# Optimization experiments

Measured on AMD Instinct MI355X. Metric: run time of the kernel, lower is better.

## Reference

```python
import jax, jax.numpy as jnp
import numpy as np

NUM_EXPERTS = 8
TOP_K = 2
D = 512
F = 2048
B, L = 4, 1024


def setup_inputs() -> dict:
    key = jax.random.key(0)
    ks = jax.random.split(key, 5)
    std = D ** -0.5
    return {
        "x": jax.random.normal(ks[0], (B, L, D), jnp.float32),
        "gate_w": jax.random.normal(ks[1], (NUM_EXPERTS, D), jnp.float32) * std,
        "w1": jax.random.normal(ks[2], (NUM_EXPERTS, F, D), jnp.float32) * std,
        "w2": jax.random.normal(ks[3], (NUM_EXPERTS, D, F), jnp.float32) * (F ** -0.5),
        "w3": jax.random.normal(ks[4], (NUM_EXPERTS, F, D), jnp.float32) * std,
    }


def reference(x, gate_w, w1, w2, w3):
    b, l, d = x.shape
    xf = x.reshape(-1, d)                      # [T, D]
    T = xf.shape[0]
    router_logits = xf @ gate_w.T              # [T, E]
    # top-k routing in float32 (as in original), softmax over selected logits
    topk_w, topk_idx = jax.lax.top_k(router_logits.astype(jnp.float32), TOP_K)
    topk_w = jax.nn.softmax(topk_w, axis=-1).astype(x.dtype)  # [T, K]
    # combine weights per (token, expert): scatter top-k weights into dense [T, E]
    cw = jnp.zeros((T, NUM_EXPERTS), x.dtype)
    cw = cw.at[jnp.arange(T)[:, None], topk_idx].add(topk_w)
    # per-expert gated FFN (SiLU(x w1^T) * (x w3^T)) w2^T, batched over experts
    h = jax.nn.silu(jnp.einsum('td,efd->etf', xf, w1)) * jnp.einsum('td,efd->etf', xf, w3)
    y = jnp.einsum('etf,edf->etd', h, w2)      # [E, T, D]
    out = jnp.einsum('te,etd->td', cw, y)      # weighted combine
    return out.reshape(b, l, d), router_logits
```

## Files before the change

### kernel.cpp

```cpp
#include <hip/hip_runtime.h>

#define TTOK 4096
#define NEXP 8
#define DDIM 512
#define FDIM 2048
#define HROWS 8576

typedef __attribute__((ext_vector_type(8))) short short8;
typedef __attribute__((ext_vector_type(4))) float floatx4;

#define BAR()  __builtin_amdgcn_s_barrier()
#define SBAR() __builtin_amdgcn_sched_barrier(0)

__device__ __forceinline__ ushort f2b(float f) {
  unsigned u = __float_as_uint(f);
  u += 0x7fffu + ((u >> 16) & 1u);
  return (ushort)(u >> 16);
}

__device__ __forceinline__ void load16(void* lds, const void* g) {
  __builtin_amdgcn_global_load_lds(
      (const __attribute__((address_space(1))) unsigned int*)g,
      (__attribute__((address_space(3))) unsigned int*)lds, 16, 0, 0);
}


__global__ __launch_bounds__(256) void k_front(
    const float* __restrict__ x, const float* __restrict__ gw,
    float* __restrict__ logits, int* __restrict__ tok_e,
    float2* __restrict__ tok_w,
    const float* __restrict__ w1, ushort* __restrict__ w1t,
    const float* __restrict__ w3, ushort* __restrict__ w3t)
{
  __shared__ ushort sm[4096];
  const int tid = threadIdx.x;
  if (blockIdx.x < TTOK / 4) {
    const int lane = tid & 63;
    const int t = blockIdx.x * 4 + (tid >> 6);
    float xv[8];
#pragma unroll
    for (int i = 0; i < 8; ++i) xv[i] = x[(size_t)t * DDIM + lane + 64 * i];
    float lg[8];
#pragma unroll
    for (int e = 0; e < 8; ++e) {
      float a = 0.f;
#pragma unroll
      for (int i = 0; i < 8; ++i) a += xv[i] * gw[e * DDIM + lane + 64 * i];
#pragma unroll
      for (int s = 32; s; s >>= 1) a += __shfl_xor(a, s, 64);
      lg[e] = a;
    }
    if (lane < 8) logits[(size_t)t * 8 + lane] = lg[lane];
    if (lane == 0) {
      int i0 = 0; float v0 = lg[0];
#pragma unroll
      for (int e = 1; e < 8; ++e) { if (lg[e] > v0) { v0 = lg[e]; i0 = e; } }
      int i1 = -1; float v1 = -3.4e38f;
#pragma unroll
      for (int e = 0; e < 8; ++e) { if (e != i0 && lg[e] > v1) { v1 = lg[e]; i1 = e; } }
      float ex = expf(v1 - v0);
      float inv = 1.f / (1.f + ex);
      tok_e[t] = i0 | (i1 << 4);
      tok_w[t] = make_float2(inv, ex * inv);
    }
    return;
  }
  int bid = blockIdx.x - TTOK / 4;
  const float* src = (bid < 2048) ? w1 : w3;
  ushort* dst = (bid < 2048) ? w1t : w3t;
  if (bid >= 2048) bid -= 2048;
  const int r0 = (bid >> 2) * 32;
  const int c0 = (bid & 3) * 128;
#pragma unroll
  for (int i = 0; i < 4; ++i) {
    int j = i * 1024 + tid * 4;
    int lr = j >> 7, lc = j & 127;
    float4 v = *(const float4*)&src[(size_t)(r0 + lr) * 512 + c0 + lc];
    ushort4 b = { f2b(v.x), f2b(v.y), f2b(v.z), f2b(v.w) };
    int ord = (lr >> 4) * 4 + (lc >> 5);
    int slot = (lr & 15) + 16 * ((lc >> 3) & 3);
    *(ushort4*)&sm[(ord * 64 + slot) * 8 + (lc & 7)] = b;
  }
  __syncthreads();
  const size_t tb0 = ((size_t)(r0 >> 4) * 16 + (c0 >> 5)) * 512;
#pragma unroll
  for (int rt = 0; rt < 2; ++rt)
    *(short8*)&dst[tb0 + (size_t)rt * 16 * 512 + tid * 8] =
        *(const short8*)&sm[rt * 2048 + tid * 8];
}

__global__ __launch_bounds__(1024) void k_build(
    const int* __restrict__ tok_e, const float2* __restrict__ tok_w,
    int* __restrict__ counts, int* __restrict__ lists, float* __restrict__ wts)
{
  const int e = blockIdx.x;
  const int tid = threadIdx.x;
  const int lane = tid & 63, wid = tid >> 6;
  __shared__ int wcnt[16];
  __shared__ int sbase;
  if (tid == 0) sbase = 0;
  __syncthreads();

  for (int c = 0; c < TTOK; c += 1024) {
    int t = c + tid;
    int pe = tok_e[t];
    bool m0 = (pe & 15) == e;
    bool m1 = ((pe >> 4) & 15) == e;
    bool m = m0 || m1;
    unsigned long long b = __ballot(m);
    int lpre = __popcll(b & ((1ull << lane) - 1ull));
    if (lane == 0) wcnt[wid] = __popcll(b);
    __syncthreads();
    int woff = 0;
#pragma unroll
    for (int i = 0; i < 16; ++i) if (i < wid) woff += wcnt[i];
    if (m) {
      float2 w = tok_w[t];
      int pos = sbase + woff + lpre;
      lists[e * TTOK + pos] = t;
      wts[e * TTOK + pos] = m0 ? w.x : w.y;
    }
    __syncthreads();
    if (tid == 0) {
      int s = 0;
#pragma unroll
      for (int i = 0; i < 16; ++i) s += wcnt[i];
      sbase += s;
    }
    __syncthreads();
  }
  if (tid == 0) counts[e] = sbase;
}

__global__ __launch_bounds__(256) void k_gather(
    const float* __restrict__ x, const int* __restrict__ counts,
    const int* __restrict__ lists, ushort* __restrict__ Xg)
{
  int pp[9];
  pp[0] = 0;
#pragma unroll
  for (int i = 0; i < 8; ++i) pp[i + 1] = pp[i] + ((counts[i] + 31) & ~31);
  int gid = blockIdx.x * 256 + threadIdx.x;
  int gr = gid >> 6, dg = gid & 63;
  if (gr >= pp[8]) return;
  int e = 0;
  while (e < 7 && gr >= pp[e + 1]) ++e;
  int p = gr - pp[e];
  size_t dst = ((size_t)(gr >> 4) * 16 + (dg >> 2)) * 512
             + ((gr & 15) + 16 * (dg & 3)) * 8;
  short8 o = (short8)0;
  if (p < counts[e]) {
    int t = lists[e * TTOK + p];
    const float* s = x + (size_t)t * DDIM + dg * 8;
    float4 a = *(const float4*)s;
    float4 b = *(const float4*)(s + 4);
    o[0] = f2b(a.x); o[1] = f2b(a.y); o[2] = f2b(a.z); o[3] = f2b(a.w);
    o[4] = f2b(b.x); o[5] = f2b(b.y); o[6] = f2b(b.z); o[7] = f2b(b.w);
  }
  *(short8*)&Xg[dst] = o;
}

__global__ __launch_bounds__(512) void k_ffn1(
    const ushort* __restrict__ Xg, const ushort* __restrict__ w1t,
    const ushort* __restrict__ w3t, const int* __restrict__ counts,
    ushort* __restrict__ H,
    const float* __restrict__ w2, ushort* __restrict__ w2t)
{
  __shared__ ushort Xls[2][4096], W1ls[2][4096], W3ls[2][4096];
  const int tid = threadIdx.x;

  if (blockIdx.x >= 4096) {
    int bid = blockIdx.x - 4096;
    ushort* sm = &Xls[0][0];
    const int r0 = (bid >> 4) * 32;
    const int c0 = (bid & 15) * 128;
#pragma unroll
    for (int i = 0; i < 2; ++i) {
      int j = i * 2048 + tid * 4;
      int lr = j >> 7, lc = j & 127;
      float4 v = *(const float4*)&w2[(size_t)(r0 + lr) * 2048 + c0 + lc];
      ushort4 b = { f2b(v.x), f2b(v.y), f2b(v.z), f2b(v.w) };
      int ord = (lr >> 4) * 4 + (lc >> 5);
      int slot = (lr & 15) + 16 * ((lc >> 3) & 3);
      *(ushort4*)&sm[(ord * 64 + slot) * 8 + (lc & 7)] = b;
    }
    __syncthreads();
    const size_t tb0 = ((size_t)(r0 >> 4) * 64 + (c0 >> 5)) * 512;
    int rt = tid >> 8, s = tid & 255;
    *(short8*)&w2t[tb0 + (size_t)rt * 64 * 512 + s * 8] =
        *(const short8*)&sm[rt * 2048 + s * 8];
    return;
  }

  const int bid = blockIdx.x;
  const int widx = (bid & 7) * 512 + (bid >> 3);
  const int mt = widx & 31, e = (widx >> 5) & 7, ft = widx >> 8;
  const int ne = counts[e];
  const int m0 = mt * 128;
  if (m0 >= ne) return;
  const int f0 = ft * 128;
  int hb = 0;
#pragma unroll
  for (int i = 0; i < 7; ++i) if (i < e) hb += (counts[i] + 31) & ~31;
  const int wid = tid >> 6, lane = tid & 63;
  const int wm = wid >> 2, wn = wid & 3;
  const int lr = lane & 15, lgp = lane >> 4;

  const int rtX0 = (hb + m0) >> 4;
  const ushort* sx = Xg  + ((size_t)(rtX0 + wid) * 16) * 512 + lane * 8;
  const ushort* s1 = w1t + ((size_t)(e * 128 + (f0 >> 4) + wid) * 16) * 512 + lane * 8;
  const ushort* s3 = w3t + ((size_t)(e * 128 + (f0 >> 4) + wid) * 16) * 512 + lane * 8;

#define FFN1_STAGE(B)                                                       \
  { load16((char*)&Xls[B][0]  + wid * 1024, sx);                            \
    load16((char*)&W1ls[B][0] + wid * 1024, s1);                            \
    load16((char*)&W3ls[B][0] + wid * 1024, s3);                            \
    sx += 512; s1 += 512; s3 += 512; }

#define FFN1_COMPUTE(B)                                                     \
  { short8 af[4], b1[2], b3[2];                                             \
    _Pragma("unroll")                                                       \
    for (int mf = 0; mf < 4; ++mf)                                          \
      af[mf] = *(const short8*)&Xls[B][(wm * 4 + mf) * 512 + lane * 8];     \
    _Pragma("unroll")                                                       \
    for (int nf = 0; nf < 2; ++nf) {                                        \
      b1[nf] = *(const short8*)&W1ls[B][(wn * 2 + nf) * 512 + lane * 8];    \
      b3[nf] = *(const short8*)&W3ls[B][(wn * 2 + nf) * 512 + lane * 8];    \
    }                                                                       \
    _Pragma("unroll")                                                       \
    for (int mf = 0; mf < 4; ++mf)                                          \
      _Pragma("unroll")                                                     \
      for (int nf = 0; nf < 2; ++nf) {                                      \
        acc1[mf][nf] = __builtin_amdgcn_mfma_f32_16x16x32_bf16(             \
            af[mf], b1[nf], acc1[mf][nf], 0, 0, 0);                         \
        acc3[mf][nf] = __builtin_amdgcn_mfma_f32_16x16x32_bf16(             \
            af[mf], b3[nf], acc3[mf][nf], 0, 0, 0);                         \
      } }

  floatx4 acc1[4][2], acc3[4][2];
#pragma unroll
  for (int a = 0; a < 4; ++a)
#pragma unroll
    for (int b = 0; b < 2; ++b) { acc1[a][b] = (floatx4)0.f; acc3[a][b] = (floatx4)0.f; }

  FFN1_STAGE(0);
  for (int t = 0; t < 16; t += 2) {
    FFN1_STAGE(1);
    asm volatile("s_waitcnt vmcnt(3)" ::: "memory");
    BAR(); SBAR();
    FFN1_COMPUTE(0);
    SBAR(); BAR();
    if (t + 2 < 16) {
      FFN1_STAGE(0);
      asm volatile("s_waitcnt vmcnt(3)" ::: "memory");
    } else {
      asm volatile("s_waitcnt vmcnt(0)" ::: "memory");
    }
    BAR(); SBAR();
    FFN1_COMPUTE(1);
    SBAR(); BAR();
  }

#pragma unroll
  for (int mf = 0; mf < 4; ++mf) {
    const int rtOut = rtX0 + wm * 4 + mf;
#pragma unroll
    for (int nf = 0; nf < 2; ++nf) {
      const int kt = (f0 >> 5) + wn;
      const int slotc = (nf * 2 + (lr >> 3)) & 3;
      size_t base = ((size_t)rtOut * 64 + kt) * 512 + 16 * slotc * 8 + (lr & 7);
      floatx4 v1 = acc1[mf][nf], v3 = acc3[mf][nf];
#pragma unroll
      for (int j = 0; j < 4; ++j) {
        int p = m0 + wm * 64 + mf * 16 + lgp * 4 + j;
        if (p < ne) {
          float h1 = v1[j], h3 = v3[j];
          float sig = 1.f / (1.f + __expf(-h1));
          H[base + (size_t)(lgp * 4 + j) * 8] = f2b(h1 * sig * h3);
        }
      }
    }
  }
#undef FFN1_STAGE
#undef FFN1_COMPUTE
}

__global__ __launch_bounds__(512) void k_ffn2(
    const ushort* __restrict__ Ht, const ushort* __restrict__ w2t,
    const int* __restrict__ counts, const int* __restrict__ lists,
    const float* __restrict__ wts, float* __restrict__ out)
{
  const int bid = blockIdx.x;
  const int widx = (bid & 7) * 256 + (bid >> 3);
  const int mt = widx & 31, e = (widx >> 5) & 7;
  const int rest = widx >> 8;
  const int dt = rest & 3, ks = rest >> 2;
  const int ne = counts[e];
  const int m0 = mt * 128;
  if (m0 >= ne) return;
  const int d0 = dt * 128;
  int hb = 0;
#pragma unroll
  for (int i = 0; i < 7; ++i) if (i < e) hb += (counts[i] + 31) & ~31;
  const int tid = threadIdx.x;
  const int wid = tid >> 6, lane = tid & 63;
  const int wm = wid >> 2, wn = wid & 3;
  const int lr = lane & 15, lgp = lane >> 4;

  __shared__ ushort Hls[2][8192], W2ls[2][8192];
  __shared__ int toks[128];
  __shared__ float twt[128];

  if (tid < 128) {
    int p = m0 + tid;
    bool v = p < ne;
    toks[tid] = v ? lists[e * TTOK + p] : 0;
    twt[tid] = v ? wts[e * TTOK + p] : 0.f;
  }

  const int rtH0 = (hb + m0) >> 4;
  const int kb = ks * 32;
  const ushort* sh = Ht  + ((size_t)(rtH0 + wid) * 64 + kb) * 512 + lane * 8;
  const ushort* sw = w2t + ((size_t)(e * 32 + (d0 >> 4) + wid) * 64 + kb) * 512 + lane * 8;

#define FFN2_STAGE(B)                                                      \
  { load16((char*)&Hls[B][0]  + (wid * 2) * 1024, sh);                     \
    load16((char*)&Hls[B][0]  + (wid * 2 + 1) * 1024, sh + 512);           \
    load16((char*)&W2ls[B][0] + (wid * 2) * 1024, sw);                     \
    load16((char*)&W2ls[B][0] + (wid * 2 + 1) * 1024, sw + 512);           \
    sh += 1024; sw += 1024; }

#define FFN2_COMPUTE(B)                                                    \
  { _Pragma("unroll")                                                      \
    for (int kk = 0; kk < 2; ++kk) {                                       \
      short8 af[4], bf[2];                                                 \
      _Pragma("unroll")                                                    \
      for (int mf = 0; mf < 4; ++mf)                                       \
        af[mf] = *(const short8*)&Hls[B][((wm * 4 + mf) * 2 + kk) * 512 + lane * 8]; \
      _Pragma("unroll")                                                    \
      for (int nf = 0; nf < 2; ++nf)                                       \
        bf[nf] = *(const short8*)&W2ls[B][((wn * 2 + nf) * 2 + kk) * 512 + lane * 8]; \
      _Pragma("unroll")                                                    \
      for (int mf = 0; mf < 4; ++mf)                                       \
        _Pragma("unroll")                                                  \
        for (int nf = 0; nf < 2; ++nf)                                     \
          acc[mf][nf] = __builtin_amdgcn_mfma_f32_16x16x32_bf16(           \
              af[mf], bf[nf], acc[mf][nf], 0, 0, 0);                       \
    } }

  floatx4 acc[4][2];
#pragma unroll
  for (int a = 0; a < 4; ++a)
#pragma unroll
    for (int b = 0; b < 2; ++b) acc[a][b] = (floatx4)0.f;

  FFN2_STAGE(0);
  for (int t = 0; t < 16; t += 2) {
    FFN2_STAGE(1);
    asm volatile("s_waitcnt vmcnt(4)" ::: "memory");
    BAR(); SBAR();
    FFN2_COMPUTE(0);
    SBAR(); BAR();
    if (t + 2 < 16) {
      FFN2_STAGE(0);
      asm volatile("s_waitcnt vmcnt(4)" ::: "memory");
    } else {
      asm volatile("s_waitcnt vmcnt(0)" ::: "memory");
    }
    BAR(); SBAR();
    FFN2_COMPUTE(1);
    SBAR(); BAR();
  }

#pragma unroll
  for (int mf = 0; mf < 4; ++mf) {
#pragma unroll
    for (int j = 0; j < 4; ++j) {
      int rloc = wm * 64 + mf * 16 + lgp * 4 + j;
      int p = m0 + rloc;
      if (p < ne) {
        int t = toks[rloc];
        float w = twt[rloc];
#pragma unroll
        for (int nf = 0; nf < 2; ++nf) {
          int d = d0 + wn * 32 + nf * 16 + lr;
          atomicAdd(&out[(size_t)t * DDIM + d], w * acc[mf][nf][j]);
        }
      }
    }
  }
#undef FFN2_STAGE
#undef FFN2_COMPUTE
}

extern "C" void kernel_launch(void* const* d_in, const int* in_sizes, int n_in,
                              void* d_out, int out_size, void* d_ws, size_t ws_size,
                              hipStream_t stream) {
  const float* x  = (const float*)d_in[0];
  const float* gw = (const float*)d_in[1];
  const float* w1 = (const float*)d_in[2];
  const float* w2 = (const float*)d_in[3];
  const float* w3 = (const float*)d_in[4];
  float* out = (float*)d_out;
  float* logits = out + (size_t)TTOK * DDIM;

  int* counts = (int*)d_ws;
  int* tok_e  = counts + 16;
  float2* tok_w = (float2*)(tok_e + TTOK);
  int* lists  = (int*)(tok_w + TTOK);
  float* wts  = (float*)(lists + NEXP * TTOK);
  ushort* w1t = (ushort*)(wts + NEXP * TTOK);
  ushort* w3t = w1t + (size_t)NEXP * FDIM * DDIM;
  ushort* w2t = w3t + (size_t)NEXP * FDIM * DDIM;
  ushort* Xg  = w2t + (size_t)NEXP * DDIM * FDIM;
  ushort* H   = Xg + (size_t)HROWS * DDIM;

  hipMemsetAsync(d_out, 0, (size_t)TTOK * DDIM * sizeof(float), stream);

  k_front<<<TTOK / 4 + 4096, 256, 0, stream>>>(x, gw, logits, tok_e, tok_w,
                                               w1, w1t, w3, w3t);
  k_build<<<NEXP, 1024, 0, stream>>>(tok_e, tok_w, counts, lists, wts);
  k_gather<<<(8448 * 64) / 256, 256, 0, stream>>>(x, counts, lists, Xg);

  k_ffn1<<<4096 + 2048, 512, 0, stream>>>(Xg, w1t, w3t, counts, H, w2, w2t);
  k_ffn2<<<2048, 512, 0, stream>>>(H, w2t, counts, lists, wts, out);
}
```

Measured before the change: 146.2 us.

## Fold output zeroing into front kernel and restructure FFN double-buffer pipeline

Drops the separate memset of the output and zeroes it inside the routing part of the front kernel, saving a launch and a pass over memory. The FFN1 and FFN2 main loops are restructured so that the next stage's loads are issued before computing the current buffer, with one full vmcnt(0) wait and barrier per stage instead of two barriers around partial waits. This halves the barrier count and allows deeper overlap. In exchange, a full vmcnt wait can stall on the just-issued loads before the buffer swap.

New measurement: 169.7 us. 16.1% more time.

```diff
diff --git a/kernel.cpp b/kernel.cpp
--- a/kernel.cpp
+++ b/kernel.cpp
@@ -11,6 +11,7 @@
 
 #define BAR()  __builtin_amdgcn_s_barrier()
 #define SBAR() __builtin_amdgcn_sched_barrier(0)
+#define VM0()  asm volatile("s_waitcnt vmcnt(0)" ::: "memory")
 
 __device__ __forceinline__ ushort f2b(float f) {
   unsigned u = __float_as_uint(f);
@@ -28,13 +29,17 @@
 __global__ __launch_bounds__(256) void k_front(
     const float* __restrict__ x, const float* __restrict__ gw,
     float* __restrict__ logits, int* __restrict__ tok_e,
-    float2* __restrict__ tok_w,
+    float2* __restrict__ tok_w, float* __restrict__ outz,
     const float* __restrict__ w1, ushort* __restrict__ w1t,
     const float* __restrict__ w3, ushort* __restrict__ w3t)
 {
   __shared__ ushort sm[4096];
   const int tid = threadIdx.x;
   if (blockIdx.x < TTOK / 4) {
+    float4 zz = {0.f, 0.f, 0.f, 0.f};
+    float4* orow = (float4*)(outz + (size_t)blockIdx.x * 4 * DDIM);
+    orow[tid] = zz;
+    orow[tid + 256] = zz;
     const int lane = tid & 63;
     const int t = blockIdx.x * 4 + (tid >> 6);
     float xv[8];
@@ -244,21 +249,14 @@
     for (int b = 0; b < 2; ++b) { acc1[a][b] = (floatx4)0.f; acc3[a][b] = (floatx4)0.f; }
 
   FFN1_STAGE(0);
+  VM0(); BAR(); SBAR();
   for (int t = 0; t < 16; t += 2) {
-    FFN1_STAGE(1);
-    asm volatile("s_waitcnt vmcnt(3)" ::: "memory");
-    BAR(); SBAR();
+    if (t + 1 < 16) FFN1_STAGE(1);
     FFN1_COMPUTE(0);
-    SBAR(); BAR();
-    if (t + 2 < 16) {
-      FFN1_STAGE(0);
-      asm volatile("s_waitcnt vmcnt(3)" ::: "memory");
-    } else {
-      asm volatile("s_waitcnt vmcnt(0)" ::: "memory");
-    }
-    BAR(); SBAR();
+    SBAR(); VM0(); BAR(); SBAR();
+    if (t + 2 < 16) FFN1_STAGE(0);
     FFN1_COMPUTE(1);
-    SBAR(); BAR();
+    SBAR(); VM0(); BAR(); SBAR();
   }
 
 #pragma unroll
@@ -355,21 +353,14 @@
     for (int b = 0; b < 2; ++b) acc[a][b] = (floatx4)0.f;
 
   FFN2_STAGE(0);
+  VM0(); BAR(); SBAR();
   for (int t = 0; t < 16; t += 2) {
-    FFN2_STAGE(1);
-    asm volatile("s_waitcnt vmcnt(4)" ::: "memory");
-    BAR(); SBAR();
+    if (t + 1 < 16) FFN2_STAGE(1);
     FFN2_COMPUTE(0);
-    SBAR(); BAR();
-    if (t + 2 < 16) {
-      FFN2_STAGE(0);
-      asm volatile("s_waitcnt vmcnt(4)" ::: "memory");
-    } else {
-      asm volatile("s_waitcnt vmcnt(0)" ::: "memory");
-    }
-    BAR(); SBAR();
+    SBAR(); VM0(); BAR(); SBAR();
+    if (t + 2 < 16) FFN2_STAGE(0);
     FFN2_COMPUTE(1);
-    SBAR(); BAR();
+    SBAR(); VM0(); BAR(); SBAR();
   }
 
 #pragma unroll
@@ -415,10 +406,8 @@
   ushort* Xg  = w2t + (size_t)NEXP * DDIM * FDIM;
   ushort* H   = Xg + (size_t)HROWS * DDIM;
 
-  hipMemsetAsync(d_out, 0, (size_t)TTOK * DDIM * sizeof(float), stream);
-
   k_front<<<TTOK / 4 + 4096, 256, 0, stream>>>(x, gw, logits, tok_e, tok_w,
-                                               w1, w1t, w3, w3t);
+                                               out, w1, w1t, w3, w3t);
   k_build<<<NEXP, 1024, 0, stream>>>(tok_e, tok_w, counts, lists, wts);
   k_gather<<<(8448 * 64) / 256, 256, 0, stream>>>(x, counts, lists, Xg);
 
```
